# Kernel optimization log

Hardware: AMD Instinct MI355X
Metric: run time of the kernel (lower is better)

The kernel has to match this reference:

```python
import jax, jax.numpy as jnp
import numpy as np

N_NODES = 50000
N_EDGES = 800000
D_IN = 128
D_SH = 16
D_OUT = 128
N_PATHS = 64


def setup_inputs() -> dict:
    key = jax.random.key(0)
    k1, k2, k3, k4, k5, k6, k7, k8 = jax.random.split(key, 8)
    x = jax.random.normal(k1, (N_NODES, D_IN), dtype=jnp.float32)
    sh = jax.random.normal(k2, (N_EDGES, D_SH), dtype=jnp.float32)
    coeff = jax.random.normal(k3, (N_PATHS,), dtype=jnp.float32)
    src = jax.random.randint(k4, (N_EDGES,), 0, N_NODES, dtype=jnp.int64)
    dst = jax.random.randint(k5, (N_EDGES,), 0, N_NODES, dtype=jnp.int64)
    ki = jax.random.randint(k6, (N_PATHS,), 0, D_IN, dtype=jnp.int32)
    kj = jax.random.randint(k7, (N_PATHS,), 0, D_SH, dtype=jnp.int32)
    ko = jax.random.randint(k8, (N_PATHS,), 0, D_OUT, dtype=jnp.int32)
    return {"x": x, "sh": sh, "coeff": coeff, "src": src, "dst": dst,
            "ki": ki, "kj": kj, "ko": ko}


def reference(x, sh, coeff, src, dst, ki, kj, ko):
    # 1) gather: index_select node features by edge source -> [E, D_in]
    xg = x[src]
    # 2) segmented tensor product: sum over sparse paths p of
    #    coeff[p] * xg[:, ki[p]] * sh[:, kj[p]] accumulated into output slot ko[p]
    vals = coeff[None, :] * xg[:, ki] * sh[:, kj]          # [E, P]
    msg = jnp.zeros((sh.shape[0], D_OUT), dtype=x.dtype).at[:, ko].add(vals)  # [E, D_out]
    # 3) scatter_add messages into per-node output -> [N, D_out]
    out = jnp.zeros((x.shape[0], D_OUT), dtype=x.dtype).at[dst].add(msg)
    return out
```

## Files before the change

kernel.cpp:

```cpp
#include <hip/hip_runtime.h>
#include <hip/hip_fp16.h>

#define N_NODES 50000
#define N_EDGES 800000
#define D_IN    128
#define D_SH    16
#define D_OUT   128
#define N_PATHS 64

#define SEGN    128
#define NSEG    391
#define NSEGP   512
#define CAPE    2560
#define EPB     3125
#define BINB    256
#define XCB     3125
#define BLK     256

#define QN      32
#define QCAP    1024
#define NQB     (NSEG * 4)

#define OFF_META 2048
#define OFF_SH16 (OFF_META + NSEG*CAPE*4)
#define OFF_XCH  (OFF_SH16 + NSEG*CAPE*32)

__global__ __launch_bounds__(BLK) void bin_kernel(
        const float* __restrict__ x, const int* __restrict__ ki,
        const float* __restrict__ sh, const int* __restrict__ src,
        const int* __restrict__ dst, int* __restrict__ segcnt,
        int* __restrict__ meta, __half* __restrict__ sh16,
        __half* __restrict__ xc_h) {
    __shared__ int lcnt[NSEGP];
    __shared__ int lstart[NSEGP];
    __shared__ int lofs[NSEGP];
    __shared__ int gbase[NSEGP];
    __shared__ unsigned short sorted_[EPB];
    const int tid = threadIdx.x;

    if (blockIdx.x < BINB) {
        const int e0 = blockIdx.x * EPB;
        for (int s = tid; s < NSEGP; s += BLK) lcnt[s] = 0;
        __syncthreads();
        for (int i = tid; i < EPB; i += BLK)
            atomicAdd(&lcnt[dst[e0 + i] >> 7], 1);
        __syncthreads();
        if (tid < 64) {
            int b8 = tid * 8, v[8], s0 = 0;
            #pragma unroll
            for (int k = 0; k < 8; ++k) { v[k] = lcnt[b8 + k]; s0 += v[k]; }
            int run = s0;
            #pragma unroll
            for (int off = 1; off < 64; off <<= 1) {
                int y = __shfl_up(run, off);
                if (tid >= off) run += y;
            }
            int acc = run - s0;
            #pragma unroll
            for (int k = 0; k < 8; ++k) {
                lstart[b8 + k] = acc; lofs[b8 + k] = acc; acc += v[k];
            }
        } else {
            for (int s = tid - 64; s < NSEG; s += BLK - 64) {
                int c = lcnt[s];
                gbase[s] = c ? atomicAdd(&segcnt[s], c) : 0;
            }
        }
        __syncthreads();
        for (int i = tid; i < EPB; i += BLK) {
            int r = atomicAdd(&lofs[dst[e0 + i] >> 7], 1);
            sorted_[r] = (unsigned short)i;
        }
        __syncthreads();
        for (int j = tid; j < EPB; j += BLK) {
            int i = sorted_[j];
            int e = e0 + i;
            int d = dst[e];
            int s = d >> 7;
            int pos = gbase[s] + (j - lstart[s]);
            if (pos < CAPE) {
                size_t gi = (size_t)s * CAPE + pos;
                meta[gi] = src[e] | ((d & 127) << 16);
                const float4* shv = (const float4*)(sh + (size_t)e * D_SH);
                float4 f0 = shv[0], f1 = shv[1], f2 = shv[2], f3 = shv[3];
                union { __half2 h[8]; int4 v[2]; } u;
                u.h[0] = __floats2half2_rn(f0.x, f0.y);
                u.h[1] = __floats2half2_rn(f0.z, f0.w);
                u.h[2] = __floats2half2_rn(f1.x, f1.y);
                u.h[3] = __floats2half2_rn(f1.z, f1.w);
                u.h[4] = __floats2half2_rn(f2.x, f2.y);
                u.h[5] = __floats2half2_rn(f2.z, f2.w);
                u.h[6] = __floats2half2_rn(f3.x, f3.y);
                u.h[7] = __floats2half2_rn(f3.z, f3.w);
                int4* dp = (int4*)(sh16 + gi * 16);
                dp[0] = u.v[0]; dp[1] = u.v[1];
            }
        }
    } else {
        const int b2   = blockIdx.x - BINB;
        const int lane = tid & 63;
        const int w    = tid >> 6;
        const int nb   = b2 * 16 + w * 4;
        const int kil  = ki[lane];
        float x0 = x[(size_t)(nb + 0) * D_IN + kil];
        float x1 = x[(size_t)(nb + 1) * D_IN + kil];
        float x2 = x[(size_t)(nb + 2) * D_IN + kil];
        float x3 = x[(size_t)(nb + 3) * D_IN + kil];
        xc_h[(size_t)(nb + 0) * N_PATHS + lane] = __float2half_rn(x0);
        xc_h[(size_t)(nb + 1) * N_PATHS + lane] = __float2half_rn(x1);
        xc_h[(size_t)(nb + 2) * N_PATHS + lane] = __float2half_rn(x2);
        xc_h[(size_t)(nb + 3) * N_PATHS + lane] = __float2half_rn(x3);
    }
}

__global__ __launch_bounds__(BLK) void node_kernel(
        const int* __restrict__ segcnt, const int* __restrict__ meta,
        const __half* __restrict__ sh16, const __half* __restrict__ xc_h,
        const float* __restrict__ coeff, const int* __restrict__ kj,
        const int* __restrict__ ko, float* __restrict__ out) {
    __shared__ int cnt_l[QN];
    __shared__ int nstart[QN + 1];
    __shared__ int ncur[QN];
    __shared__ unsigned short csr_src[QCAP];
    __shared__ unsigned short csr_idx[QCAP];
    __shared__ float srow[BLK / 64][D_OUT];
    const int tid  = threadIdx.x;
    const int lane = tid & 63;
    const int w    = tid >> 6;
    const int seg  = blockIdx.x >> 2;
    const int q    = blockIdx.x & 3;
    const int nb_l = q * QN;
    const int n_e  = min(segcnt[seg], CAPE);
    const size_t mb = (size_t)seg * CAPE;
    const __half* shb = sh16 + mb * 16;

    if (tid < QN) cnt_l[tid] = 0;
    __syncthreads();
    for (int i = tid; i < n_e; i += BLK) {
        unsigned int u = (unsigned)(((meta[mb + i] >> 16) & 127) - nb_l);
        if (u < QN) atomicAdd(&cnt_l[u], 1);
    }
    __syncthreads();
    if (tid < QN) {
        int v = cnt_l[tid];
        int run = v;
        #pragma unroll
        for (int off = 1; off < QN; off <<= 1) {
            int y = __shfl_up(run, off);
            if (tid >= off) run += y;
        }
        nstart[tid] = run - v;
        ncur[tid]   = run - v;
        if (tid == QN - 1) nstart[QN] = run;
    }
    __syncthreads();
    for (int i = tid; i < n_e; i += BLK) {
        int m = meta[mb + i];
        unsigned int u = (unsigned)(((m >> 16) & 127) - nb_l);
        if (u < QN) {
            int r = atomicAdd(&ncur[u], 1);
            if (r < QCAP) {
                csr_src[r] = (unsigned short)(m & 0xFFFF);
                csr_idx[r] = (unsigned short)i;
            }
        }
    }
    __syncthreads();

    const int   kj_p = kj[lane];
    const int   ko_p = ko[lane];
    const float c_p  = coeff[lane];

    #pragma unroll 1
    for (int k = 0; k < QN / (BLK / 64); ++k) {
        const int c    = w * (QN / (BLK / 64)) + k;
        const int node = seg * SEGN + nb_l + c;
        const int st   = nstart[c];
        const int en   = nstart[c + 1];
        float acc = 0.0f;
        int j = st;
        for (; j + 8 <= en; j += 8) {
            float xv[8], sv[8];
            #pragma unroll
            for (int u8 = 0; u8 < 8; ++u8) {
                int s = csr_src[j + u8];
                int i = csr_idx[j + u8];
                xv[u8] = __half2float(xc_h[(size_t)s * N_PATHS + lane]);
                sv[u8] = __half2float(shb[(size_t)i * 16 + kj_p]);
            }
            #pragma unroll
            for (int u8 = 0; u8 < 8; ++u8) acc += xv[u8] * sv[u8];
        }
        if (j < en) {
            float xv[8], sv[8];
            #pragma unroll
            for (int u8 = 0; u8 < 8; ++u8) {
                int jj = j + u8;
                int jc = jj < en ? jj : st;
                int s = csr_src[jc];
                int i = csr_idx[jc];
                xv[u8] = __half2float(xc_h[(size_t)s * N_PATHS + lane]);
                sv[u8] = __half2float(shb[(size_t)i * 16 + kj_p]);
            }
            #pragma unroll
            for (int u8 = 0; u8 < 8; ++u8)
                if (j + u8 < en) acc += xv[u8] * sv[u8];
        }
        acc *= c_p;
        if (node < N_NODES) {
            srow[w][lane]      = 0.0f;
            srow[w][lane + 64] = 0.0f;
            atomicAdd(&srow[w][ko_p], acc);
            float r0 = srow[w][lane];
            float r1 = srow[w][lane + 64];
            float* orow = out + (size_t)node * D_OUT;
            orow[lane]      = r0;
            orow[lane + 64] = r1;
        }
    }
}

extern "C" void kernel_launch(void* const* d_in, const int* in_sizes, int n_in,
                              void* d_out, int out_size, void* d_ws, size_t ws_size,
                              hipStream_t stream) {
    const float* x     = (const float*)d_in[0];
    const float* sh    = (const float*)d_in[1];
    const float* coeff = (const float*)d_in[2];
    const int*   src   = (const int*)d_in[3];
    const int*   dst   = (const int*)d_in[4];
    const int*   ki    = (const int*)d_in[5];
    const int*   kj    = (const int*)d_in[6];
    const int*   ko    = (const int*)d_in[7];
    float* out = (float*)d_out;

    char* p = (char*)d_ws;
    int*    segcnt = (int*)p;
    int*    meta   = (int*)(p + OFF_META);
    __half* sh16   = (__half*)(p + OFF_SH16);
    __half* xc_h   = (__half*)(p + OFF_XCH);
    (void)ws_size;

    hipMemsetAsync(segcnt, 0, 2048, stream);
    bin_kernel<<<BINB + XCB, BLK, 0, stream>>>(
        x, ki, sh, src, dst, segcnt, meta, sh16, xc_h);
    node_kernel<<<NQB, BLK, 0, stream>>>(
        segcnt, meta, sh16, xc_h, coeff, kj, ko, out);
}
```

Before: 208.5 us.

## Split node segments into eighths, cache meta in registers, widen gather unroll

Each 128-node segment is now handled by eight blocks of 16 nodes instead of four blocks of 32, which doubles the number of blocks and gives each wave four nodes. Each thread loads the segment's meta entries once into registers and reuses them for both the count pass and the CSR-build pass, so meta is no longer read twice per block. The gather loop is unrolled to 16 edges to keep more loads in flight. The per-node shared-memory reduction by output slot is batched across the four nodes. The cost is that every segment's meta is now scanned by eight blocks instead of four, and the larger unroll plus register cache raises register pressure.

```diff
diff --git a/kernel.cpp b/kernel.cpp
--- a/kernel.cpp
+++ b/kernel.cpp
@@ -17,9 +17,10 @@
 #define XCB     3125
 #define BLK     256
 
-#define QN      32
-#define QCAP    1024
-#define NQB     (NSEG * 4)
+#define QN      16
+#define QCAP    512
+#define NQB     (NSEG * 8)
+#define SCAN_K  10
 
 #define OFF_META 2048
 #define OFF_SH16 (OFF_META + NSEG*CAPE*4)
@@ -123,12 +124,12 @@
     __shared__ int ncur[QN];
     __shared__ unsigned short csr_src[QCAP];
     __shared__ unsigned short csr_idx[QCAP];
-    __shared__ float srow[BLK / 64][D_OUT];
+    __shared__ float srow[BLK / 64][4][D_OUT];
     const int tid  = threadIdx.x;
     const int lane = tid & 63;
     const int w    = tid >> 6;
-    const int seg  = blockIdx.x >> 2;
-    const int q    = blockIdx.x & 3;
+    const int seg  = blockIdx.x >> 3;
+    const int q    = blockIdx.x & 7;
     const int nb_l = q * QN;
     const int n_e  = min(segcnt[seg], CAPE);
     const size_t mb = (size_t)seg * CAPE;
@@ -136,9 +137,15 @@
 
     if (tid < QN) cnt_l[tid] = 0;
     __syncthreads();
-    for (int i = tid; i < n_e; i += BLK) {
-        unsigned int u = (unsigned)(((meta[mb + i] >> 16) & 127) - nb_l);
-        if (u < QN) atomicAdd(&cnt_l[u], 1);
+
+    int mreg[SCAN_K];
+    #pragma unroll
+    for (int k = 0; k < SCAN_K; ++k) {
+        int i = tid + k * BLK;
+        int m = (i < n_e) ? meta[mb + i] : -1;
+        mreg[k] = m;
+        unsigned int u = (unsigned)(((m >> 16) & 127) - nb_l);
+        if (i < n_e && u < QN) atomicAdd(&cnt_l[u], 1);
     }
     __syncthreads();
     if (tid < QN) {
@@ -154,10 +161,12 @@
         if (tid == QN - 1) nstart[QN] = run;
     }
     __syncthreads();
-    for (int i = tid; i < n_e; i += BLK) {
-        int m = meta[mb + i];
+    #pragma unroll
+    for (int k = 0; k < SCAN_K; ++k) {
+        int i = tid + k * BLK;
+        int m = mreg[k];
         unsigned int u = (unsigned)(((m >> 16) & 127) - nb_l);
-        if (u < QN) {
+        if (i < n_e && u < QN) {
             int r = atomicAdd(&ncur[u], 1);
             if (r < QCAP) {
                 csr_src[r] = (unsigned short)(m & 0xFFFF);
@@ -171,30 +180,30 @@
     const int   ko_p = ko[lane];
     const float c_p  = coeff[lane];
 
-    #pragma unroll 1
-    for (int k = 0; k < QN / (BLK / 64); ++k) {
-        const int c    = w * (QN / (BLK / 64)) + k;
-        const int node = seg * SEGN + nb_l + c;
-        const int st   = nstart[c];
-        const int en   = nstart[c + 1];
+    float accs[4];
+    #pragma unroll
+    for (int c4 = 0; c4 < 4; ++c4) {
+        const int c  = w * 4 + c4;
+        const int st = min(nstart[c], QCAP);
+        const int en = min(nstart[c + 1], QCAP);
         float acc = 0.0f;
         int j = st;
-        for (; j + 8 <= en; j += 8) {
-            float xv[8], sv[8];
-            #pragma unroll
-            for (int u8 = 0; u8 < 8; ++u8) {
+        for (; j + 16 <= en; j += 16) {
+            float xv[16], sv[16];
+            #pragma unroll
+            for (int u8 = 0; u8 < 16; ++u8) {
                 int s = csr_src[j + u8];
                 int i = csr_idx[j + u8];
                 xv[u8] = __half2float(xc_h[(size_t)s * N_PATHS + lane]);
                 sv[u8] = __half2float(shb[(size_t)i * 16 + kj_p]);
             }
             #pragma unroll
-            for (int u8 = 0; u8 < 8; ++u8) acc += xv[u8] * sv[u8];
+            for (int u8 = 0; u8 < 16; ++u8) acc += xv[u8] * sv[u8];
         }
         if (j < en) {
-            float xv[8], sv[8];
-            #pragma unroll
-            for (int u8 = 0; u8 < 8; ++u8) {
+            float xv[16], sv[16];
+            #pragma unroll
+            for (int u8 = 0; u8 < 16; ++u8) {
                 int jj = j + u8;
                 int jc = jj < en ? jj : st;
                 int s = csr_src[jc];
@@ -203,16 +212,26 @@
                 sv[u8] = __half2float(shb[(size_t)i * 16 + kj_p]);
             }
             #pragma unroll
-            for (int u8 = 0; u8 < 8; ++u8)
+            for (int u8 = 0; u8 < 16; ++u8)
                 if (j + u8 < en) acc += xv[u8] * sv[u8];
         }
-        acc *= c_p;
+        accs[c4] = acc * c_p;
+    }
+
+    #pragma unroll
+    for (int c4 = 0; c4 < 4; ++c4) {
+        srow[w][c4][lane]      = 0.0f;
+        srow[w][c4][lane + 64] = 0.0f;
+    }
+    #pragma unroll
+    for (int c4 = 0; c4 < 4; ++c4)
+        atomicAdd(&srow[w][c4][ko_p], accs[c4]);
+    #pragma unroll
+    for (int c4 = 0; c4 < 4; ++c4) {
+        const int node = seg * SEGN + nb_l + w * 4 + c4;
         if (node < N_NODES) {
-            srow[w][lane]      = 0.0f;
-            srow[w][lane + 64] = 0.0f;
-            atomicAdd(&srow[w][ko_p], acc);
-            float r0 = srow[w][lane];
-            float r1 = srow[w][lane + 64];
+            float r0 = srow[w][c4][lane];
+            float r1 = srow[w][c4][lane + 64];
             float* orow = out + (size_t)node * D_OUT;
             orow[lane]      = r0;
             orow[lane + 64] = r1;
```

Result: slower. 216.2 us (+3.7%).
